# Kernel tuning notes

Measured on AMD Instinct MI355X. Metric: run time of the kernel, lower is better.

The kernel has to match this reference:

```python
import jax, jax.numpy as jnp
import numpy as np

EPS = 1e-5
CUT = 5.0  # ExpNormalSmearing cutoff_upper (cutoff_lower = 0)


def _smearing(dist, means, betas):
    # ExpNormalSmearing with CosineCutoff
    alpha = 5.0 / CUT
    cutoff = 0.5 * (jnp.cos(dist * jnp.pi / CUT) + 1.0) * (dist < CUT)
    return cutoff * jnp.exp(-betas * (jnp.exp(-alpha * dist) - means) ** 2)


def setup_inputs() -> dict:
    B, N, F, HID, HEADS, K = 2, 512, 32, 32, 4, 50
    C = HEADS * HID
    key = jax.random.key(0)
    ks = jax.random.split(key, 24)
    d = lambda k, i, o: jax.random.normal(k, (i, o), jnp.float32) / np.sqrt(i)
    z = lambda n: jnp.zeros((n,), jnp.float32)
    start = float(np.exp(-CUT))
    return dict(
        h=jax.random.normal(ks[0], (B, N, F), jnp.float32),
        x=jax.random.normal(ks[1], (B, N, 3), jnp.float32),
        v=jax.random.normal(ks[2], (B, N, 3), jnp.float32) * 0.1,
        means=jnp.linspace(start, 1.0, K, dtype=jnp.float32),
        betas=jnp.full((K,), (2.0 / K * (1.0 - start)) ** -2, jnp.float32),
        W_in=d(ks[3], 2 * F, K), b_in=z(K),
        W_o1=d(ks[4], 2 * F + K + 1, HID), b_o1=z(HID),
        W_o2=d(ks[5], HID, HID), b_o2=z(HID),
        W_sem=d(ks[6], HID, HEADS), b_sem=z(HEADS),
        W_pn1=d(ks[7], C, HID), b_pn1=z(HID),
        W_pn2=d(ks[8], HID, HID), b_pn2=z(HID),
        W_n1=d(ks[9], F + C + HID, HID), b_n1=z(HID),
        W_n2=d(ks[10], HID, F), b_n2=z(F),
        W_v1=d(ks[11], F, HID), b_v1=z(HID),
        W_v2=d(ks[12], HID, 1) * 0.001,
        W_vm=d(ks[13], C, 1),
        log_gamma=-jnp.log(jnp.linspace(1.0, 5.0, HEADS)).astype(jnp.float32),
    )


def reference(h, x, v, means, betas, W_in, b_in, W_o1, b_o1, W_o2, b_o2,
              W_sem, b_sem, W_pn1, b_pn1, W_pn2, b_pn2, W_n1, b_n1, W_n2, b_n2,
              W_v1, b_v1, W_v2, W_vm, log_gamma):
    silu = jax.nn.silu
    B, N, F = h.shape
    HID = W_o2.shape[-1]
    HEADS = W_sem.shape[-1]

    # pairwise geometry: x_minus_xt[b,i,j] = x[b,j] - x[b,i]
    x_minus_xt = x[:, None, :, :] - x[:, :, None, :]                    # (B,N,N,3)
    norm = (jax.nn.relu((x_minus_xt ** 2).sum(-1, keepdims=True)) + EPS) ** 0.5  # (B,N,N,1)

    # pair features: [h_j ; h_i]
    h_cat_ht = jnp.concatenate([
        jnp.broadcast_to(h[:, None, :, :], (B, N, N, F)),
        jnp.broadcast_to(h[:, :, None, :], (B, N, N, F)),
    ], axis=-1)                                                         # (B,N,N,2F)

    # edge model (ContinuousFilterConvolutionWithConcatenation)
    hk = h_cat_ht @ W_in + b_in                                         # (B,N,N,K)
    _x = _smearing(norm, means, betas) * hk
    h_e_mtx = silu(jnp.concatenate([h_cat_ht, _x, norm], -1) @ W_o1 + b_o1) @ W_o2 + b_o2  # (B,N,N,HID)

    # dual attention (softmax over j = axis -2), self-pairs masked by +/-1e5
    eye = jnp.eye(N, dtype=h.dtype)[:, :, None]                         # (N,N,1)
    eucl = jax.nn.softmax(-(norm + 1e5 * eye) * jnp.exp(log_gamma), axis=-2)   # (B,N,N,HEADS)
    sem = jax.nn.leaky_relu(h_e_mtx @ W_sem + b_sem, negative_slope=0.2)
    sem = jax.nn.softmax(sem - 1e5 * eye, axis=-2)
    comb = jax.nn.softmax(eucl * sem, axis=-2)                          # (B,N,N,HEADS)

    # attended edge features, (HID, HEADS) flattened -> C = HID*HEADS
    h_e_att = (h_e_mtx[..., :, None] * comb[..., None, :]).reshape(B, N, N, HID * HEADS)

    # spatial attention: combinations[b,i,j,c,d] = unit[b,i,j,d]*h_e_att[b,i,j,c],
    # immediately reduced over j -> fuse into einsum (no (B,N,N,C,3) intermediate)
    unit = x_minus_xt / (norm + EPS)
    comb_sum = jnp.einsum('bijc,bijd->bicd', h_e_att, unit) / N         # mean over j, (B,N,C,3)
    h_comb = (comb_sum ** 2).sum(-1)                                    # (B,N,C)
    h_comb = silu(silu(h_comb @ W_pn1 + b_pn1) @ W_pn2 + b_pn2)
    # v_mixing over C then mean over j == contraction of comb_sum with W_vm
    delta_v = jnp.einsum('bicd,co->bid', comb_sum, W_vm)                # (B,N,3)

    # aggregate + node model (residual)
    h_e = h_e_att.sum(axis=-2)                                          # (B,N,C)
    out = jnp.concatenate([h, h_e, h_comb], -1)
    h_new = h + silu(silu(out @ W_n1 + b_n1) @ W_n2 + b_n2)

    # velocity + position update
    v_new = (silu(h_new @ W_v1 + b_v1) @ W_v2) * v + delta_v
    x_new = x + v_new
    return h_new, x_new, v_new
```

## Files before the change

kernel.cpp:

```cpp
#include <hip/hip_runtime.h>
#include <hip/hip_bf16.h>

#define BB 2
#define NN 512
#define FF 32
#define HH 32
#define NH 4
#define KK 50
#define CC 128
#define BN (BB*NN)

#define SHE 520
#define SCB 516

#define O_H      0
#define O_X      32768
#define O_V      35840
#define O_MEANS  38912
#define O_BETAS  38962
#define O_WIN    39012
#define O_BIN    42212
#define O_WO1    42262
#define O_BO1    45942
#define O_WO2    45974
#define O_BO2    46998
#define O_WSEM   47030
#define O_BSEM   47158
#define O_WPN1   47162
#define O_BPN1   51258
#define O_WPN2   51290
#define O_BPN2   52314
#define O_WN1    52346
#define O_BN1    58490
#define O_WN2    58522
#define O_BN2    59546
#define O_WV1    59578
#define O_BV1    60602
#define O_WV2    60634
#define O_WVM    60666
#define O_LGAMMA 60794
#define O_PP     60800
#define O_PQ     (O_PP + KK*BN)
#define O_PR     (O_PQ + BN*KK)
#define O_PS     (O_PR + HH*BN)

__device__ __forceinline__ float bfb2f(unsigned int hi){
  union { unsigned int u; float f; } c; c.u = hi << 16; return c.f;
}
__device__ __forceinline__ float lo16(unsigned u){
  union { unsigned x; float f; } c; c.x = u << 16; return c.f;
}
__device__ __forceinline__ float hi16(unsigned u){
  union { unsigned x; float f; } c; c.x = u & 0xffff0000u; return c.f;
}
__device__ __forceinline__ unsigned short f2bfb(float f){
  union { float f; unsigned int u; } c; c.f = f;
  unsigned int u = c.u + (0x7fffu + ((c.u >> 16) & 1u));
  return (unsigned short)(u >> 16);
}
__device__ __forceinline__ unsigned pk2(float a, float b){
  return (unsigned)f2bfb(a) | ((unsigned)f2bfb(b) << 16);
}
__device__ __forceinline__ float siluf(float x){ return x / (1.f + __expf(-x)); }
__device__ __forceinline__ bool detect_f32(const void* means_raw){
  const unsigned w0 = *(const unsigned*)means_raw;
  return ((w0 >> 16) & 0x7fffu) < 0x3C00u;
}

struct Ptrs26 { const void* p[26]; };

__global__ __launch_bounds__(256) void k_convert(Ptrs26 P, float* __restrict__ dst)
{
  static const int SZ[26]  = {32768,3072,3072,50,50,3200,50,3680,32,1024,32,128,4,
                              4096,32,1024,32,6144,32,1024,32,1024,32,32,128,4};
  static const int OFFT[26] = {O_H,O_X,O_V,O_MEANS,O_BETAS,O_WIN,O_BIN,O_WO1,O_BO1,
                              O_WO2,O_BO2,O_WSEM,O_BSEM,O_WPN1,O_BPN1,O_WPN2,O_BPN2,
                              O_WN1,O_BN1,O_WN2,O_BN2,O_WV1,O_BV1,O_WV2,O_WVM,O_LGAMMA};
  static const int CA[34] = {0,0,0,0,0,0,0,0, 1,2,3,4,5,6,7,8,9,10,11,12,13,14,15,16,
                             17,17, 18,19,20,21,22,23,24,25};
  static const int CO[34] = {0,4096,8192,12288,16384,20480,24576,28672,
                             0,0,0,0,0,0,0,0,0,0,0,0,0,0,0,0, 0,4096,
                             0,0,0,0,0,0,0,0};
  const bool f32 = detect_f32(P.p[3]);
  const int ch = blockIdx.x;
  const int ai = CA[ch], off = CO[ch];
  const int n = min(4096, SZ[ai] - off);
  float* d = dst + OFFT[ai] + off;
  if (f32) {
    const float* s = (const float*)P.p[ai] + off;
    for (int e = threadIdx.x; e < n; e += 256) d[e] = s[e];
  } else {
    const unsigned short* s = (const unsigned short*)P.p[ai] + off;
    for (int e = threadIdx.x; e < n; e += 256) d[e] = bfb2f((unsigned)s[e]);
  }
}

__global__ __launch_bounds__(256) void k_pre(const float* __restrict__ W,
    float* __restrict__ pP, float* __restrict__ pQ,
    float* __restrict__ pR, float* __restrict__ pS)
{
  __shared__ float hrow[FF];
  const int node = blockIdx.x;
  const int tid = threadIdx.x;
  if (tid < FF) hrow[tid] = W[O_H + node*FF + tid];
  __syncthreads();
  if (tid < KK) {
    float a = 0.f;
    for (int f = 0; f < FF; ++f) a = fmaf(hrow[f], W[O_WIN + f*KK + tid], a);
    pP[tid*BN + node] = a;
  } else if (tid < 2*KK) {
    const int k = tid - KK;
    float a = W[O_BIN + k];
    for (int f = 0; f < FF; ++f) a = fmaf(hrow[f], W[O_WIN + (FF+f)*KK + k], a);
    pQ[node*KK + k] = a;
  } else if (tid < 2*KK + HH) {
    const int m = tid - 2*KK;
    float a = 0.f;
    for (int f = 0; f < FF; ++f) a = fmaf(hrow[f], W[O_WO1 + f*HH + m], a);
    pR[m*BN + node] = a;
  } else if (tid < 2*KK + 2*HH) {
    const int m = tid - 2*KK - HH;
    float a = W[O_BO1 + m];
    for (int f = 0; f < FF; ++f) a = fmaf(hrow[f], W[O_WO1 + (FF+f)*HH + m], a);
    pS[node*HH + m] = a;
  }
}

__device__ __forceinline__ void red8sum(float* a, volatile float* sRed, int lane, int wid)
{
  #pragma unroll
  for (int o = 32; o > 0; o >>= 1) {
    #pragma unroll
    for (int v = 0; v < 8; ++v) a[v] += __shfl_xor(a[v], o);
  }
  __syncthreads();
  if (lane == 0) {
    #pragma unroll
    for (int v = 0; v < 8; ++v) sRed[wid*8+v] = a[v];
  }
  __syncthreads();
  #pragma unroll
  for (int v = 0; v < 8; ++v) {
    float s = sRed[v];
    #pragma unroll
    for (int w = 1; w < 8; ++w) s += sRed[w*8+v];
    a[v] = s;
  }
}
__device__ __forceinline__ void red4sum(float* a, volatile float* sRed, int lane, int wid)
{
  #pragma unroll
  for (int o = 32; o > 0; o >>= 1) {
    #pragma unroll
    for (int v = 0; v < 4; ++v) a[v] += __shfl_xor(a[v], o);
  }
  __syncthreads();
  if (lane == 0) {
    #pragma unroll
    for (int v = 0; v < 4; ++v) sRed[wid*4+v] = a[v];
  }
  __syncthreads();
  #pragma unroll
  for (int v = 0; v < 4; ++v) {
    float s = sRed[v];
    #pragma unroll
    for (int w = 1; w < 8; ++w) s += sRed[w*4+v];
    a[v] = s;
  }
}

__global__ __launch_bounds__(512, 4) void k_fused(const float* __restrict__ W,
    const float* __restrict__ pP, const float* __restrict__ pQ,
    const float* __restrict__ pR, const float* __restrict__ pS,
    const void* __restrict__ rawMeans, void* __restrict__ outv)
{
  __shared__ unsigned short sHET[HH*SHE];
  __shared__ __align__(16) float sCbT[NH*SCB];
  __shared__ __align__(16) float sUT[3*NN];
  __shared__ __align__(16) unsigned sPartU[4*CC*2];
  __shared__ float sRed[64];

  float* pool   = (float*)sPartU;
  float* sHraw  = pool;
  float* sCS    = pool + 128;
  float* sOut   = pool + 512;
  float* sT1    = pool + 704;
  float* sT2    = pool + 736;
  float* sDv    = pool + 768;
  float* sScale = pool + 771;

  const int node = blockIdx.x;
  const int b    = node >> 9;
  const int ii   = node & (NN - 1);
  const int tid  = threadIdx.x;
  const int lane = tid & 63, wid = tid >> 6;
  const bool f32out = detect_f32(rawMeans);

  const int j = tid;
  const int nbj = b*NN + j;

  const float xi0 = W[O_X + node*3 + 0];
  const float xi1 = W[O_X + node*3 + 1];
  const float xi2 = W[O_X + node*3 + 2];

  const float dx = W[O_X + nbj*3+0] - xi0;
  const float dy = W[O_X + nbj*3+1] - xi1;
  const float dz = W[O_X + nbj*3+2] - xi2;
  const float d2 = fmaxf(dx*dx + dy*dy + dz*dz, 0.f);
  const float nrm = sqrtf(d2 + 1e-5f);
  const float invd = 1.f / (nrm + 1e-5f);
  sUT[0*NN + j] = dx*invd;
  sUT[1*NN + j] = dy*invd;
  sUT[2*NN + j] = dz*invd;

  const float cutoff = (nrm < 5.0f) ? (0.5f * (__cosf(nrm * 0.628318530717958647692f) + 1.0f)) : 0.f;
  const float e_d = __expf(-nrm);

  float acc[HH];
  #pragma unroll
  for (int m = 0; m < HH; ++m)
    acc[m] = pR[m*BN + nbj] + pS[node*HH + m] + nrm * W[O_WO1 + (2*FF+KK)*HH + m];

  {
    const float mu0 = W[O_MEANS + 0];
    const float mu1 = W[O_MEANS + 1];
    const float beta = W[O_BETAS + 0];
    const float del = mu1 - mu0;
    const float t0 = e_d - mu0;
    const float t1 = e_d - mu1;
    float E  = -beta*t0*t0;
    float dE = (-beta*t1*t1) - E;
    const float c2 = -2.f*beta*del*del;
    #pragma unroll 2
    for (int k = 0; k < KK; ++k) {
      const float c = cutoff * __expf(E) * (pP[k*BN + nbj] + pQ[node*KK + k]);
      E += dE; dE += c2;
      #pragma unroll
      for (int m = 0; m < HH; ++m)
        acc[m] = fmaf(c, W[O_WO1 + (2*FF + k)*HH + m], acc[m]);
    }
  }

  float he[HH];
  #pragma unroll
  for (int q = 0; q < HH; ++q) he[q] = W[O_BO2 + q];
  #pragma unroll
  for (int m = 0; m < HH; ++m) {
    const float cs = siluf(acc[m]);
    #pragma unroll
    for (int q = 0; q < HH; ++q)
      he[q] = fmaf(cs, W[O_WO2 + m*HH + q], he[q]);
  }

  float sl0 = W[O_BSEM+0], sl1 = W[O_BSEM+1], sl2 = W[O_BSEM+2], sl3 = W[O_BSEM+3];
  #pragma unroll
  for (int q = 0; q < HH; ++q) {
    const float c = he[q];
    sl0 = fmaf(c, W[O_WSEM + q*NH + 0], sl0);
    sl1 = fmaf(c, W[O_WSEM + q*NH + 1], sl1);
    sl2 = fmaf(c, W[O_WSEM + q*NH + 2], sl2);
    sl3 = fmaf(c, W[O_WSEM + q*NH + 3], sl3);
  }
  sl0 = sl0 >= 0.f ? sl0 : 0.2f*sl0;
  sl1 = sl1 >= 0.f ? sl1 : 0.2f*sl1;
  sl2 = sl2 >= 0.f ? sl2 : 0.2f*sl2;
  sl3 = sl3 >= 0.f ? sl3 : 0.2f*sl3;

  #pragma unroll
  for (int q = 0; q < HH; ++q) sHET[q*SHE + j] = f2bfb(he[q]);

  const float msk = (j == ii) ? 1e5f : 0.f;
  const float g0 = __expf(W[O_LGAMMA+0]), g1 = __expf(W[O_LGAMMA+1]);
  const float g2 = __expf(W[O_LGAMMA+2]), g3 = __expf(W[O_LGAMMA+3]);

  const float nm = nrm + msk;
  float r8[8];
  const float es0 = __expf(sl0 - msk), es1 = __expf(sl1 - msk);
  const float es2 = __expf(sl2 - msk), es3 = __expf(sl3 - msk);
  const float eu0 = __expf(-nm*g0), eu1 = __expf(-nm*g1);
  const float eu2 = __expf(-nm*g2), eu3 = __expf(-nm*g3);
  r8[0]=es0; r8[1]=es1; r8[2]=es2; r8[3]=es3;
  r8[4]=eu0; r8[5]=eu1; r8[6]=eu2; r8[7]=eu3;
  red8sum(r8, sRed, lane, wid);

  float r4[4];
  r4[0] = __expf((es0/r8[0])*(eu0/r8[4]));
  r4[1] = __expf((es1/r8[1])*(eu1/r8[5]));
  r4[2] = __expf((es2/r8[2])*(eu2/r8[6]));
  r4[3] = __expf((es3/r8[3])*(eu3/r8[7]));
  const float cb0 = r4[0], cb1 = r4[1], cb2 = r4[2], cb3 = r4[3];
  red4sum(r4, sRed, lane, wid);
  sCbT[0*SCB + j] = cb0/r4[0];
  sCbT[1*SCB + j] = cb1/r4[1];
  sCbT[2*SCB + j] = cb2/r4[2];
  sCbT[3*SCB + j] = cb3/r4[3];
  __syncthreads();

  {
    const int c = tid & (CC-1);
    const int part = tid >> 7;
    const int q = c >> 2, hd = c & 3;
    float eA = 0.f, c0 = 0.f, c1 = 0.f, c2a = 0.f;
    const unsigned short* heRow = &sHET[q*SHE + part*128];
    const float* cbRow = &sCbT[hd*SCB + part*128];
    const float* u0Row = &sUT[0*NN + part*128];
    const float* u1Row = &sUT[1*NN + part*128];
    const float* u2Row = &sUT[2*NN + part*128];
    for (int t8 = 0; t8 < 16; ++t8) {
      const uint4 hb = *(const uint4*)(heRow + t8*8);
      const float4 cA = *(const float4*)(cbRow + t8*8);
      const float4 cB = *(const float4*)(cbRow + t8*8 + 4);
      const float4 a0 = *(const float4*)(u0Row + t8*8);
      const float4 b0 = *(const float4*)(u0Row + t8*8 + 4);
      const float4 a1 = *(const float4*)(u1Row + t8*8);
      const float4 b1 = *(const float4*)(u1Row + t8*8 + 4);
      const float4 a2 = *(const float4*)(u2Row + t8*8);
      const float4 b2 = *(const float4*)(u2Row + t8*8 + 4);
      float p;
      p = lo16(hb.x)*cA.x; eA += p; c0 = fmaf(p,a0.x,c0); c1 = fmaf(p,a1.x,c1); c2a = fmaf(p,a2.x,c2a);
      p = hi16(hb.x)*cA.y; eA += p; c0 = fmaf(p,a0.y,c0); c1 = fmaf(p,a1.y,c1); c2a = fmaf(p,a2.y,c2a);
      p = lo16(hb.y)*cA.z; eA += p; c0 = fmaf(p,a0.z,c0); c1 = fmaf(p,a1.z,c1); c2a = fmaf(p,a2.z,c2a);
      p = hi16(hb.y)*cA.w; eA += p; c0 = fmaf(p,a0.w,c0); c1 = fmaf(p,a1.w,c1); c2a = fmaf(p,a2.w,c2a);
      p = lo16(hb.z)*cB.x; eA += p; c0 = fmaf(p,b0.x,c0); c1 = fmaf(p,b1.x,c1); c2a = fmaf(p,b2.x,c2a);
      p = hi16(hb.z)*cB.y; eA += p; c0 = fmaf(p,b0.y,c0); c1 = fmaf(p,b1.y,c1); c2a = fmaf(p,b2.y,c2a);
      p = lo16(hb.w)*cB.z; eA += p; c0 = fmaf(p,b0.z,c0); c1 = fmaf(p,b1.z,c1); c2a = fmaf(p,b2.z,c2a);
      p = hi16(hb.w)*cB.w; eA += p; c0 = fmaf(p,b0.w,c0); c1 = fmaf(p,b1.w,c1); c2a = fmaf(p,b2.w,c2a);
    }
    *reinterpret_cast<uint2*>(&sPartU[(part*CC + c)*2]) =
        make_uint2(pk2(eA, c0), pk2(c1, c2a));
  }
  __syncthreads();
  uint2 pr[4];
  if (tid < CC) {
    #pragma unroll
    for (int p = 0; p < 4; ++p)
      pr[p] = *reinterpret_cast<const uint2*>(&sPartU[(p*CC + tid)*2]);
  }
  __syncthreads();
  if (tid < CC) {
    float e = 0.f, d0 = 0.f, d1 = 0.f, d2v = 0.f;
    #pragma unroll
    for (int p = 0; p < 4; ++p) {
      e   += lo16(pr[p].x); d0 += hi16(pr[p].x);
      d1  += lo16(pr[p].y); d2v += hi16(pr[p].y);
    }
    const float invN = 1.f / (float)NN;
    d0 *= invN; d1 *= invN; d2v *= invN;
    sCS[tid*3+0] = d0; sCS[tid*3+1] = d1; sCS[tid*3+2] = d2v;
    sOut[FF + tid] = e;
    sHraw[tid] = d0*d0 + d1*d1 + d2v*d2v;
  }
  if (tid < FF) sOut[tid] = W[O_H + node*FF + tid];
  __syncthreads();

  if (tid < HH) {
    float a = W[O_BPN1 + tid];
    for (int c = 0; c < CC; ++c) a = fmaf(sHraw[c], W[O_WPN1 + c*HH + tid], a);
    sT1[tid] = siluf(a);
  } else if (tid >= 64 && tid < 67) {
    const int d = tid - 64;
    float a = 0.f;
    for (int c = 0; c < CC; ++c) a = fmaf(sCS[c*3 + d], W[O_WVM + c], a);
    sDv[d] = a;
  }
  __syncthreads();
  if (tid < HH) {
    float a = W[O_BPN2 + tid];
    for (int m = 0; m < HH; ++m) a = fmaf(sT1[m], W[O_WPN2 + m*HH + tid], a);
    sOut[FF + CC + tid] = siluf(a);
  }
  __syncthreads();
  if (tid < HH) {
    float a = W[O_BN1 + tid];
    for (int r = 0; r < FF + CC + HH; ++r) a = fmaf(sOut[r], W[O_WN1 + r*HH + tid], a);
    sT1[tid] = siluf(a);
  }
  __syncthreads();
  if (tid < FF) {
    float a = W[O_BN2 + tid];
    for (int m = 0; m < HH; ++m) a = fmaf(sT1[m], W[O_WN2 + m*FF + tid], a);
    const float hn = sOut[tid] + siluf(a);
    sT2[tid] = hn;
    if (f32out) ((float*)outv)[node*FF + tid] = hn;
    else ((unsigned short*)outv)[node*FF + tid] = f2bfb(hn);
  }
  __syncthreads();
  if (tid < HH) {
    float a = W[O_BV1 + tid];
    for (int m = 0; m < FF; ++m) a = fmaf(sT2[m], W[O_WV1 + m*HH + tid], a);
    sT1[tid] = siluf(a);
  }
  __syncthreads();
  if (tid == 0) {
    float a = 0.f;
    for (int m = 0; m < HH; ++m) a = fmaf(sT1[m], W[O_WV2 + m], a);
    sScale[0] = a;
  }
  __syncthreads();
  if (tid < 3) {
    const float vv = W[O_V + node*3 + tid];
    const float vn = sScale[0]*vv + sDv[tid];
    const float xn = ((tid==0)?xi0:(tid==1)?xi1:xi2) + vn;
    if (f32out) {
      ((float*)outv)[BN*FF + node*3 + tid] = xn;
      ((float*)outv)[BN*FF + BN*3 + node*3 + tid] = vn;
    } else {
      ((unsigned short*)outv)[BN*FF + node*3 + tid] = f2bfb(xn);
      ((unsigned short*)outv)[BN*FF + BN*3 + node*3 + tid] = f2bfb(vn);
    }
  }
}

extern "C" void kernel_launch(void* const* d_in, const int* in_sizes, int n_in,
                              void* d_out, int out_size, void* d_ws, size_t ws_size,
                              hipStream_t stream) {
  (void)in_sizes; (void)n_in; (void)out_size; (void)ws_size;
  float* Wc = (float*)d_ws;
  float* pP = Wc + O_PP;
  float* pQ = Wc + O_PQ;
  float* pR = Wc + O_PR;
  float* pS = Wc + O_PS;

  Ptrs26 P;
  for (int i = 0; i < 26; ++i) P.p[i] = d_in[i];

  k_convert<<<34, 256, 0, stream>>>(P, Wc);
  k_pre<<<BN, 256, 0, stream>>>(Wc, pP, pQ, pR, pS);
  k_fused<<<BN, 512, 0, stream>>>(Wc, pP, pQ, pR, pS, d_in[3], d_out);
}
```

Measured before the change: 199.9 us.

## Move per-edge MLP to bf16 MFMA and fold W_o2·W_sem into one matrix

The per-edge hidden layers (edge MLP layer 1 with RBF, h_j, distance and bias columns, layer 2, and the semantic head) are now computed with 16x16x32 bf16 MFMA tiles staged in LDS instead of scalar FMA loops per thread. An extra k_pre block precomputes W_o2·W_sem and the folded bias, so the attention logits come from a single extra MFMA. The attended aggregation now reduces directly from MFMA accumulator registers using cross-lane shuffles plus a small LDS reduction, replacing the old transposed-LDS pass. This trades a large amount of VALU work for matrix-core throughput. The costs are extra bf16 rounding of the activations and weights, a 64KB LDS footprint that may lower occupancy, and reliance on lgkmcnt waits rather than barriers in places.

```diff
diff --git a/kernel.cpp b/kernel.cpp
--- a/kernel.cpp
+++ b/kernel.cpp
@@ -9,9 +9,6 @@
 #define KK 50
 #define CC 128
 #define BN (BB*NN)
-
-#define SHE 520
-#define SCB 516
 
 #define O_H      0
 #define O_X      32768
@@ -41,8 +38,12 @@
 #define O_LGAMMA 60794
 #define O_PP     60800
 #define O_PQ     (O_PP + KK*BN)
-#define O_PR     (O_PQ + BN*KK)
-#define O_PS     (O_PR + HH*BN)
+#define O_WOS    (O_PQ + BN*KK)
+#define O_BOS    (O_WOS + 128)
+#define O_PS     (O_WOS + HH*BN)
+
+typedef __attribute__((ext_vector_type(8))) short bf8v;
+typedef __attribute__((ext_vector_type(4))) float f4v;
 
 __device__ __forceinline__ float bfb2f(unsigned int hi){
   union { unsigned int u; float f; } c; c.u = hi << 16; return c.f;
@@ -95,13 +96,26 @@
   }
 }
 
-__global__ __launch_bounds__(256) void k_pre(const float* __restrict__ W,
-    float* __restrict__ pP, float* __restrict__ pQ,
-    float* __restrict__ pR, float* __restrict__ pS)
+__global__ __launch_bounds__(256) void k_pre(float* __restrict__ W,
+    float* __restrict__ pP, float* __restrict__ pQ, float* __restrict__ pS)
 {
+  const int tid = threadIdx.x;
+  if (blockIdx.x == BN) {
+    if (tid < 128) {
+      const int m = tid >> 2, hd = tid & 3;
+      float a = 0.f;
+      for (int q = 0; q < HH; ++q) a = fmaf(W[O_WO2 + m*HH + q], W[O_WSEM + q*NH + hd], a);
+      W[O_WOS + m*4 + hd] = a;
+    } else if (tid < 132) {
+      const int hd = tid - 128;
+      float a = W[O_BSEM + hd];
+      for (int q = 0; q < HH; ++q) a = fmaf(W[O_BO2 + q], W[O_WSEM + q*NH + hd], a);
+      W[O_BOS + hd] = a;
+    }
+    return;
+  }
   __shared__ float hrow[FF];
   const int node = blockIdx.x;
-  const int tid = threadIdx.x;
   if (tid < FF) hrow[tid] = W[O_H + node*FF + tid];
   __syncthreads();
   if (tid < KK) {
@@ -115,11 +129,6 @@
     pQ[node*KK + k] = a;
   } else if (tid < 2*KK + HH) {
     const int m = tid - 2*KK;
-    float a = 0.f;
-    for (int f = 0; f < FF; ++f) a = fmaf(hrow[f], W[O_WO1 + f*HH + m], a);
-    pR[m*BN + node] = a;
-  } else if (tid < 2*KK + 2*HH) {
-    const int m = tid - 2*KK - HH;
     float a = W[O_BO1 + m];
     for (int f = 0; f < FF; ++f) a = fmaf(hrow[f], W[O_WO1 + (FF+f)*HH + m], a);
     pS[node*HH + m] = a;
@@ -169,18 +178,26 @@
   }
 }
 
+#define MFMA16(a,b,c) __builtin_amdgcn_mfma_f32_16x16x32_bf16((a),(b),(c),0,0,0)
+
 __global__ __launch_bounds__(512, 4) void k_fused(const float* __restrict__ W,
     const float* __restrict__ pP, const float* __restrict__ pQ,
-    const float* __restrict__ pR, const float* __restrict__ pS,
+    const float* __restrict__ pS,
     const void* __restrict__ rawMeans, void* __restrict__ outv)
 {
-  __shared__ unsigned short sHET[HH*SHE];
-  __shared__ __align__(16) float sCbT[NH*SCB];
-  __shared__ __align__(16) float sUT[3*NN];
-  __shared__ __align__(16) unsigned sPartU[4*CC*2];
-  __shared__ float sRed[64];
-
-  float* pool   = (float*)sPartU;
+  __shared__ __align__(16) unsigned char sLDS[64000];
+
+  unsigned short* sXS  = (unsigned short*)(sLDS);
+  unsigned short* sBT1 = (unsigned short*)(sLDS + 40960);
+  unsigned short* sBT2 = (unsigned short*)(sLDS + 47616);
+  unsigned short* sBTos= (unsigned short*)(sLDS + 50176);
+  float*          sSemT= (float*)(sLDS + 40960);
+  float*          sCbT = (float*)(sLDS + 51456);
+  unsigned short* sUTb = (unsigned short*)(sLDS + 59648);
+  float*          sRed = (float*)(sLDS + 63744);
+  float*          sPartF = (float*)(sLDS);
+
+  float* pool   = sCbT;
   float* sHraw  = pool;
   float* sCS    = pool + 128;
   float* sOut   = pool + 512;
@@ -194,95 +211,144 @@
   const int ii   = node & (NN - 1);
   const int tid  = threadIdx.x;
   const int lane = tid & 63, wid = tid >> 6;
+  const int ln   = lane & 15, quad = lane >> 4, q8 = quad * 8;
+  const int jb   = wid * 64;
   const bool f32out = detect_f32(rawMeans);
 
-  const int j = tid;
-  const int nbj = b*NN + j;
-
-  const float xi0 = W[O_X + node*3 + 0];
-  const float xi1 = W[O_X + node*3 + 1];
-  const float xi2 = W[O_X + node*3 + 2];
-
+  const int j = tid, nbj = b*NN + j;
+  const float xi0 = W[O_X + node*3+0], xi1 = W[O_X + node*3+1], xi2 = W[O_X + node*3+2];
   const float dx = W[O_X + nbj*3+0] - xi0;
   const float dy = W[O_X + nbj*3+1] - xi1;
   const float dz = W[O_X + nbj*3+2] - xi2;
-  const float d2 = fmaxf(dx*dx + dy*dy + dz*dz, 0.f);
-  const float nrm = sqrtf(d2 + 1e-5f);
+  const float nrm = sqrtf(fmaxf(dx*dx + dy*dy + dz*dz, 0.f) + 1e-5f);
   const float invd = 1.f / (nrm + 1e-5f);
-  sUT[0*NN + j] = dx*invd;
-  sUT[1*NN + j] = dy*invd;
-  sUT[2*NN + j] = dz*invd;
+  ((unsigned*)sUTb)[j*2+0] = pk2(dx*invd, dy*invd);
+  ((unsigned*)sUTb)[j*2+1] = pk2(dz*invd, 0.f);
 
   const float cutoff = (nrm < 5.0f) ? (0.5f * (__cosf(nrm * 0.628318530717958647692f) + 1.0f)) : 0.f;
   const float e_d = __expf(-nrm);
 
-  float acc[HH];
-  #pragma unroll
-  for (int m = 0; m < HH; ++m)
-    acc[m] = pR[m*BN + nbj] + pS[node*HH + m] + nrm * W[O_WO1 + (2*FF+KK)*HH + m];
-
+  for (int idx = tid; idx < 32*96; idx += 512) {
+    const int m = idx & 31, kk = idx >> 5;
+    float v;
+    if (kk < KK)           v = W[O_WO1 + (2*FF + kk)*HH + m];
+    else if (kk < KK + FF) v = W[O_WO1 + (kk - KK)*HH + m];
+    else if (kk == 82)     v = W[O_WO1 + (2*FF + KK)*HH + m];
+    else if (kk == 83)     v = pS[node*HH + m];
+    else                   v = 0.f;
+    sBT1[m*104 + kk] = f2bfb(v);
+  }
+  for (int idx = tid; idx < 32*32; idx += 512) {
+    const int q = idx & 31, m = idx >> 5;
+    sBT2[q*40 + m] = f2bfb(W[O_WO2 + m*HH + q]);
+  }
+  { const int n = tid >> 5, m = tid & 31;
+    sBTos[n*40 + m] = (n < 4) ? f2bfb(W[O_WOS + m*4 + n]) : (unsigned short)0; }
+  __syncthreads();
+
+  f4v acc1[4][2];
+  #pragma unroll
+  for (int a = 0; a < 4; ++a) { acc1[a][0] = (f4v){0.f,0.f,0.f,0.f}; acc1[a][1] = (f4v){0.f,0.f,0.f,0.f}; }
+
+  float E, dE, c2r;
   {
-    const float mu0 = W[O_MEANS + 0];
-    const float mu1 = W[O_MEANS + 1];
-    const float beta = W[O_BETAS + 0];
-    const float del = mu1 - mu0;
-    const float t0 = e_d - mu0;
-    const float t1 = e_d - mu1;
-    float E  = -beta*t0*t0;
-    float dE = (-beta*t1*t1) - E;
-    const float c2 = -2.f*beta*del*del;
-    #pragma unroll 2
-    for (int k = 0; k < KK; ++k) {
-      const float c = cutoff * __expf(E) * (pP[k*BN + nbj] + pQ[node*KK + k]);
-      E += dE; dE += c2;
-      #pragma unroll
-      for (int m = 0; m < HH; ++m)
-        acc[m] = fmaf(c, W[O_WO1 + (2*FF + k)*HH + m], acc[m]);
-    }
-  }
-
-  float he[HH];
-  #pragma unroll
-  for (int q = 0; q < HH; ++q) he[q] = W[O_BO2 + q];
-  #pragma unroll
-  for (int m = 0; m < HH; ++m) {
-    const float cs = siluf(acc[m]);
-    #pragma unroll
-    for (int q = 0; q < HH; ++q)
-      he[q] = fmaf(cs, W[O_WO2 + m*HH + q], he[q]);
-  }
-
-  float sl0 = W[O_BSEM+0], sl1 = W[O_BSEM+1], sl2 = W[O_BSEM+2], sl3 = W[O_BSEM+3];
-  #pragma unroll
-  for (int q = 0; q < HH; ++q) {
-    const float c = he[q];
-    sl0 = fmaf(c, W[O_WSEM + q*NH + 0], sl0);
-    sl1 = fmaf(c, W[O_WSEM + q*NH + 1], sl1);
-    sl2 = fmaf(c, W[O_WSEM + q*NH + 2], sl2);
-    sl3 = fmaf(c, W[O_WSEM + q*NH + 3], sl3);
-  }
-  sl0 = sl0 >= 0.f ? sl0 : 0.2f*sl0;
-  sl1 = sl1 >= 0.f ? sl1 : 0.2f*sl1;
-  sl2 = sl2 >= 0.f ? sl2 : 0.2f*sl2;
-  sl3 = sl3 >= 0.f ? sl3 : 0.2f*sl3;
-
-  #pragma unroll
-  for (int q = 0; q < HH; ++q) sHET[q*SHE + j] = f2bfb(he[q]);
-
+    const float mu0 = W[O_MEANS+0], mu1 = W[O_MEANS+1], beta = W[O_BETAS+0];
+    const float del = mu1 - mu0, t0 = e_d - mu0, t1 = e_d - mu1;
+    E = -beta*t0*t0; dE = (-beta*t1*t1) - E; c2r = -2.f*beta*del*del;
+  }
+  unsigned* xsrow = (unsigned*)(sXS + j*40);
+
+  #pragma unroll
+  for (int ch = 0; ch < 3; ++ch) {
+    __asm__ volatile("s_waitcnt lgkmcnt(0)" ::: "memory");
+    #pragma unroll
+    for (int kp = 0; kp < 16; ++kp) {
+      float vv[2];
+      #pragma unroll
+      for (int h2 = 0; h2 < 2; ++h2) {
+        const int k = ch*32 + 2*kp + h2;
+        float v;
+        if (k < KK) { v = cutoff * __expf(E) * (pP[k*BN + nbj] + pQ[node*KK + k]); E += dE; dE += c2r; }
+        else if (k < KK + FF) v = W[O_H + nbj*FF + (k - KK)];
+        else if (k == 82) v = nrm;
+        else if (k == 83) v = 1.f;
+        else v = 0.f;
+        vv[h2] = v;
+      }
+      xsrow[kp] = pk2(vv[0], vv[1]);
+    }
+    __asm__ volatile("s_waitcnt lgkmcnt(0)" ::: "memory");
+    const bf8v bw0 = *(const bf8v*)&sBT1[(     ln)*104 + ch*32 + q8];
+    const bf8v bw1 = *(const bf8v*)&sBT1[(16 + ln)*104 + ch*32 + q8];
+    #pragma unroll
+    for (int tj = 0; tj < 4; ++tj) {
+      const bf8v av = *(const bf8v*)&sXS[(jb + tj*16 + ln)*40 + q8];
+      acc1[tj][0] = MFMA16(av, bw0, acc1[tj][0]);
+      acc1[tj][1] = MFMA16(av, bw1, acc1[tj][1]);
+    }
+  }
+
+  __asm__ volatile("s_waitcnt lgkmcnt(0)" ::: "memory");
+  #pragma unroll
+  for (int tj = 0; tj < 4; ++tj)
+    #pragma unroll
+    for (int tm = 0; tm < 2; ++tm)
+      #pragma unroll
+      for (int r = 0; r < 4; ++r)
+        sXS[(jb + tj*16 + quad*4 + r)*40 + tm*16 + ln] = f2bfb(siluf(acc1[tj][tm][r]));
+  __asm__ volatile("s_waitcnt lgkmcnt(0)" ::: "memory");
+
+  const float bo2a = W[O_BO2 + ln], bo2b = W[O_BO2 + 16 + ln];
+  const float bosr = W[O_BOS + (ln & 3)];
+  const float bosv = (ln < 4) ? bosr : 0.f;
+  f4v acc2[4][2], acc3[4];
+  #pragma unroll
+  for (int a = 0; a < 4; ++a) {
+    acc2[a][0] = (f4v){bo2a,bo2a,bo2a,bo2a};
+    acc2[a][1] = (f4v){bo2b,bo2b,bo2b,bo2b};
+    acc3[a]    = (f4v){bosv,bosv,bosv,bosv};
+  }
+  {
+    const bf8v b2a = *(const bf8v*)&sBT2[(     ln)*40 + q8];
+    const bf8v b2b = *(const bf8v*)&sBT2[(16 + ln)*40 + q8];
+    const bf8v bos = *(const bf8v*)&sBTos[ln*40 + q8];
+    #pragma unroll
+    for (int tj = 0; tj < 4; ++tj) {
+      const bf8v a2 = *(const bf8v*)&sXS[(jb + tj*16 + ln)*40 + q8];
+      acc2[tj][0] = MFMA16(a2, b2a, acc2[tj][0]);
+      acc2[tj][1] = MFMA16(a2, b2b, acc2[tj][1]);
+      acc3[tj]    = MFMA16(a2, bos, acc3[tj]);
+    }
+  }
+
+  __syncthreads();
+  if (ln < 4) {
+    #pragma unroll
+    for (int tj = 0; tj < 4; ++tj)
+      #pragma unroll
+      for (int r = 0; r < 4; ++r)
+        sSemT[ln*NN + jb + tj*16 + quad*4 + r] = acc3[tj][r];
+  }
+  __asm__ volatile("s_waitcnt lgkmcnt(0)" ::: "memory");
+
+  float sl[4];
+  #pragma unroll
+  for (int hd = 0; hd < 4; ++hd) {
+    const float s = sSemT[hd*NN + j];
+    sl[hd] = s >= 0.f ? s : 0.2f*s;
+  }
   const float msk = (j == ii) ? 1e5f : 0.f;
   const float g0 = __expf(W[O_LGAMMA+0]), g1 = __expf(W[O_LGAMMA+1]);
   const float g2 = __expf(W[O_LGAMMA+2]), g3 = __expf(W[O_LGAMMA+3]);
-
   const float nm = nrm + msk;
   float r8[8];
-  const float es0 = __expf(sl0 - msk), es1 = __expf(sl1 - msk);
-  const float es2 = __expf(sl2 - msk), es3 = __expf(sl3 - msk);
+  const float es0 = __expf(sl[0] - msk), es1 = __expf(sl[1] - msk);
+  const float es2 = __expf(sl[2] - msk), es3 = __expf(sl[3] - msk);
   const float eu0 = __expf(-nm*g0), eu1 = __expf(-nm*g1);
   const float eu2 = __expf(-nm*g2), eu3 = __expf(-nm*g3);
   r8[0]=es0; r8[1]=es1; r8[2]=es2; r8[3]=es3;
   r8[4]=eu0; r8[5]=eu1; r8[6]=eu2; r8[7]=eu3;
   red8sum(r8, sRed, lane, wid);
-
   float r4[4];
   r4[0] = __expf((es0/r8[0])*(eu0/r8[4]));
   r4[1] = __expf((es1/r8[1])*(eu1/r8[5]));
@@ -290,67 +356,65 @@
   r4[3] = __expf((es3/r8[3])*(eu3/r8[7]));
   const float cb0 = r4[0], cb1 = r4[1], cb2 = r4[2], cb3 = r4[3];
   red4sum(r4, sRed, lane, wid);
-  sCbT[0*SCB + j] = cb0/r4[0];
-  sCbT[1*SCB + j] = cb1/r4[1];
-  sCbT[2*SCB + j] = cb2/r4[2];
-  sCbT[3*SCB + j] = cb3/r4[3];
-  __syncthreads();
-
+  *(float4*)&sCbT[j*4] = make_float4(cb0/r4[0], cb1/r4[1], cb2/r4[2], cb3/r4[3]);
+  __asm__ volatile("s_waitcnt lgkmcnt(0)" ::: "memory");
+
+  float pacc[2][4][4] = {};
+  #pragma unroll
+  for (int tj = 0; tj < 4; ++tj) {
+    #pragma unroll
+    for (int r = 0; r < 4; ++r) {
+      const int jr = jb + tj*16 + quad*4 + r;
+      const float4 cb = *(const float4*)&sCbT[jr*4];
+      const uint2 uu = *(const uint2*)&sUTb[jr*4];
+      const float u0 = lo16(uu.x), u1 = hi16(uu.x), u2 = lo16(uu.y);
+      #pragma unroll
+      for (int tm = 0; tm < 2; ++tm) {
+        const float hev = acc2[tj][tm][r];
+        const float p0 = hev*cb.x, p1 = hev*cb.y, p2 = hev*cb.z, p3 = hev*cb.w;
+        pacc[tm][0][0] += p0; pacc[tm][0][1] = fmaf(p0,u0,pacc[tm][0][1]);
+        pacc[tm][0][2] = fmaf(p0,u1,pacc[tm][0][2]); pacc[tm][0][3] = fmaf(p0,u2,pacc[tm][0][3]);
+        pacc[tm][1][0] += p1; pacc[tm][1][1] = fmaf(p1,u0,pacc[tm][1][1]);
+        pacc[tm][1][2] = fmaf(p1,u1,pacc[tm][1][2]); pacc[tm][1][3] = fmaf(p1,u2,pacc[tm][1][3]);
+        pacc[tm][2][0] += p2; pacc[tm][2][1] = fmaf(p2,u0,pacc[tm][2][1]);
+        pacc[tm][2][2] = fmaf(p2,u1,pacc[tm][2][2]); pacc[tm][2][3] = fmaf(p2,u2,pacc[tm][2][3]);
+        pacc[tm][3][0] += p3; pacc[tm][3][1] = fmaf(p3,u0,pacc[tm][3][1]);
+        pacc[tm][3][2] = fmaf(p3,u1,pacc[tm][3][2]); pacc[tm][3][3] = fmaf(p3,u2,pacc[tm][3][3]);
+      }
+    }
+  }
+  #pragma unroll
+  for (int tm = 0; tm < 2; ++tm)
+    #pragma unroll
+    for (int hd = 0; hd < 4; ++hd)
+      #pragma unroll
+      for (int v = 0; v < 4; ++v) {
+        float t = pacc[tm][hd][v];
+        t += __shfl_xor(t, 16); t += __shfl_xor(t, 32);
+        pacc[tm][hd][v] = t;
+      }
+  if (quad == 0) {
+    #pragma unroll
+    for (int tm = 0; tm < 2; ++tm)
+      #pragma unroll
+      for (int hd = 0; hd < 4; ++hd)
+        *(float4*)&sPartF[(wid*32 + tm*16 + ln)*20 + hd*4] =
+            make_float4(pacc[tm][hd][0], pacc[tm][hd][1], pacc[tm][hd][2], pacc[tm][hd][3]);
+  }
+  __syncthreads();
   {
-    const int c = tid & (CC-1);
-    const int part = tid >> 7;
-    const int q = c >> 2, hd = c & 3;
-    float eA = 0.f, c0 = 0.f, c1 = 0.f, c2a = 0.f;
-    const unsigned short* heRow = &sHET[q*SHE + part*128];
-    const float* cbRow = &sCbT[hd*SCB + part*128];
-    const float* u0Row = &sUT[0*NN + part*128];
-    const float* u1Row = &sUT[1*NN + part*128];
-    const float* u2Row = &sUT[2*NN + part*128];
-    for (int t8 = 0; t8 < 16; ++t8) {
-      const uint4 hb = *(const uint4*)(heRow + t8*8);
-      const float4 cA = *(const float4*)(cbRow + t8*8);
-      const float4 cB = *(const float4*)(cbRow + t8*8 + 4);
-      const float4 a0 = *(const float4*)(u0Row + t8*8);
-      const float4 b0 = *(const float4*)(u0Row + t8*8 + 4);
-      const float4 a1 = *(const float4*)(u1Row + t8*8);
-      const float4 b1 = *(const float4*)(u1Row + t8*8 + 4);
-      const float4 a2 = *(const float4*)(u2Row + t8*8);
-      const float4 b2 = *(const float4*)(u2Row + t8*8 + 4);
-      float p;
-      p = lo16(hb.x)*cA.x; eA += p; c0 = fmaf(p,a0.x,c0); c1 = fmaf(p,a1.x,c1); c2a = fmaf(p,a2.x,c2a);
-      p = hi16(hb.x)*cA.y; eA += p; c0 = fmaf(p,a0.y,c0); c1 = fmaf(p,a1.y,c1); c2a = fmaf(p,a2.y,c2a);
-      p = lo16(hb.y)*cA.z; eA += p; c0 = fmaf(p,a0.z,c0); c1 = fmaf(p,a1.z,c1); c2a = fmaf(p,a2.z,c2a);
-      p = hi16(hb.y)*cA.w; eA += p; c0 = fmaf(p,a0.w,c0); c1 = fmaf(p,a1.w,c1); c2a = fmaf(p,a2.w,c2a);
-      p = lo16(hb.z)*cB.x; eA += p; c0 = fmaf(p,b0.x,c0); c1 = fmaf(p,b1.x,c1); c2a = fmaf(p,b2.x,c2a);
-      p = hi16(hb.z)*cB.y; eA += p; c0 = fmaf(p,b0.y,c0); c1 = fmaf(p,b1.y,c1); c2a = fmaf(p,b2.y,c2a);
-      p = lo16(hb.w)*cB.z; eA += p; c0 = fmaf(p,b0.z,c0); c1 = fmaf(p,b1.z,c1); c2a = fmaf(p,b2.z,c2a);
-      p = hi16(hb.w)*cB.w; eA += p; c0 = fmaf(p,b0.w,c0); c1 = fmaf(p,b1.w,c1); c2a = fmaf(p,b2.w,c2a);
-    }
-    *reinterpret_cast<uint2*>(&sPartU[(part*CC + c)*2]) =
-        make_uint2(pk2(eA, c0), pk2(c1, c2a));
-  }
-  __syncthreads();
-  uint2 pr[4];
-  if (tid < CC) {
-    #pragma unroll
-    for (int p = 0; p < 4; ++p)
-      pr[p] = *reinterpret_cast<const uint2*>(&sPartU[(p*CC + tid)*2]);
-  }
-  __syncthreads();
-  if (tid < CC) {
-    float e = 0.f, d0 = 0.f, d1 = 0.f, d2v = 0.f;
-    #pragma unroll
-    for (int p = 0; p < 4; ++p) {
-      e   += lo16(pr[p].x); d0 += hi16(pr[p].x);
-      d1  += lo16(pr[p].y); d2v += hi16(pr[p].y);
-    }
-    const float invN = 1.f / (float)NN;
-    d0 *= invN; d1 *= invN; d2v *= invN;
-    sCS[tid*3+0] = d0; sCS[tid*3+1] = d1; sCS[tid*3+2] = d2v;
-    sOut[FF + tid] = e;
-    sHraw[tid] = d0*d0 + d1*d1 + d2v*d2v;
-  }
-  if (tid < FF) sOut[tid] = W[O_H + node*FF + tid];
+    const int q = tid >> 4, g = tid & 15;
+    float s = 0.f;
+    #pragma unroll
+    for (int w = 0; w < 8; ++w) s += sPartF[(w*32 + q)*20 + g];
+    const int c = q*4 + (g >> 2), val = g & 3;
+    if (val == 0) sOut[FF + c] = s;
+    else sCS[c*3 + val - 1] = s * (1.f/512.f);
+    if (tid < FF) sOut[tid] = W[O_H + node*FF + tid];
+  }
+  __syncthreads();
+  if (tid < CC)
+    sHraw[tid] = sCS[tid*3]*sCS[tid*3] + sCS[tid*3+1]*sCS[tid*3+1] + sCS[tid*3+2]*sCS[tid*3+2];
   __syncthreads();
 
   if (tid < HH) {
@@ -418,13 +482,12 @@
   float* Wc = (float*)d_ws;
   float* pP = Wc + O_PP;
   float* pQ = Wc + O_PQ;
-  float* pR = Wc + O_PR;
   float* pS = Wc + O_PS;
 
   Ptrs26 P;
   for (int i = 0; i < 26; ++i) P.p[i] = d_in[i];
 
   k_convert<<<34, 256, 0, stream>>>(P, Wc);
-  k_pre<<<BN, 256, 0, stream>>>(Wc, pP, pQ, pR, pS);
-  k_fused<<<BN, 512, 0, stream>>>(Wc, pP, pQ, pR, pS, d_in[3], d_out);
-}
+  k_pre<<<BN + 1, 256, 0, stream>>>(Wc, pP, pQ, pS);
+  k_fused<<<BN, 512, 0, stream>>>(Wc, pP, pQ, pS, d_in[3], d_out);
+}
```

Result: faster. 180.0 us (-9.9%).
